# Performance work log

Hardware: AMD Instinct MI355X
Metric: run time of the kernel (lower is better)

## Reference

```python
import jax, jax.numpy as jnp
import numpy as np

B, H, C, HID, WIN, K = 8, 64, 128, 512, 4, 3
L = H * H

def _conv(x, w, groups, pad):
    return jax.lax.conv_general_dilated(
        x, w, (1, 1), [(pad, pad), (pad, pad)],
        dimension_numbers=('NCHW', 'OIHW', 'NCHW'), feature_group_count=groups)

def _ln(x, g, b):
    m = x.mean(-1, keepdims=True)
    v = ((x - m) ** 2).mean(-1, keepdims=True)
    return (x - m) * jax.lax.rsqrt(v + 1e-5) * g + b

def _gelu(x):
    return jax.nn.gelu(x, approximate=False)  # torch nn.GELU default = erf

def setup_inputs() -> dict:
    key = jax.random.key(0)
    ks = jax.random.split(key, 16)
    n = lambda i, sh: jax.random.normal(ks[i], sh, jnp.float32) * 0.02
    return dict(
        x=jax.random.normal(ks[0], (B, L, C), jnp.float32),
        ln1_g=jnp.ones((C,), jnp.float32), ln1_b=jnp.zeros((C,), jnp.float32),
        conv1_w=n(1, (WIN * C, C, K, K)),
        w_down=n(2, (WIN, C)), b_down=jnp.zeros((WIN,), jnp.float32),
        w1=n(3, (4 * WIN, WIN)), b1=jnp.zeros((4 * WIN,), jnp.float32),
        w2=n(4, (WIN, 4 * WIN)), b2=jnp.zeros((WIN,), jnp.float32),
        w_gk=n(5, (C, WIN * C)), b_gk=jnp.zeros((C,), jnp.float32),
        w_fus=n(6, (C, (WIN + 1) * C)), b_fus=jnp.zeros((C,), jnp.float32),
        ln2_g=jnp.ones((C,), jnp.float32), ln2_b=jnp.zeros((C,), jnp.float32),
        lin1_w=n(7, (HID, C)), lin1_b=jnp.zeros((HID,), jnp.float32),
        dw_w=n(8, (HID, 1, K, K)), dw_b=jnp.zeros((HID,), jnp.float32),
        lin2_w=n(9, (C, HID)), lin2_b=jnp.zeros((C,), jnp.float32),
    )

def _kernel_attn(x, conv1_w, w_down, b_down, w1, b1, w2, b2, w_gk, b_gk, w_fus, b_fus):
    ws = H // 2  # window grid is 2x2 since win_num=4
    xw = x.reshape(B, 2, ws, 2, ws, C).transpose(0, 1, 3, 5, 2, 4).reshape(B, WIN * C, ws, ws)
    wc = _conv(xw, conv1_w, WIN, 1)
    # WinKernel_Reweight (SE over windows)
    pooled = wc.mean((2, 3)).reshape(B, WIN, C)
    y = jnp.einsum('bgc,gc->bg', pooled, w_down) + b_down
    y = _gelu(y @ w1.T + b1)
    wgt = jax.nn.sigmoid(y @ w2.T + b2)
    k0 = conv1_w.reshape(WIN, C, C, K, K)
    kern = wgt[:, :, None, None, None, None] * k0[None]
    k_in = kern.transpose(0, 2, 1, 3, 4, 5).reshape(B * C, WIN * C, K, K)
    gk = jnp.einsum('om,nmij->noij', w_gk, k_in) + b_gk[None, :, None, None]
    kernels = jnp.concatenate([kern, gk.reshape(B, 1, C, C, K, K)], axis=1)
    kernels = kernels.reshape(B * (WIN + 1) * C, C, K, K)
    # per-sample dynamic grouped conv over full-resolution image
    ximg = x.reshape(B, H, H, C).transpose(0, 3, 1, 2)     # [B, C, H, W]
    xrep = jnp.tile(ximg, (1, WIN + 1, 1, 1)).reshape(1, B * (WIN + 1) * C, H, H)
    out = _conv(xrep, kernels, B * (WIN + 1), 1).reshape(B, (WIN + 1) * C, H, H)
    out = jnp.einsum('oc,bchw->bohw', w_fus, out) + b_fus[None, :, None, None]
    return out.transpose(0, 2, 3, 1).reshape(B, L, C)

def _leff(x, lin1_w, lin1_b, dw_w, dw_b, lin2_w, lin2_b):
    h = _gelu(x @ lin1_w.T + lin1_b)                       # [B, L, HID]
    h = h.reshape(B, H, H, HID).transpose(0, 3, 1, 2)
    h = _gelu(_conv(h, dw_w, HID, 1) + dw_b[None, :, None, None])  # depthwise 3x3
    h = h.transpose(0, 2, 3, 1).reshape(B, L, HID)
    return h @ lin2_w.T + lin2_b

def reference(x, ln1_g, ln1_b, conv1_w, w_down, b_down, w1, b1, w2, b2,
              w_gk, b_gk, w_fus, b_fus, ln2_g, ln2_b,
              lin1_w, lin1_b, dw_w, dw_b, lin2_w, lin2_b):
    x = x + _kernel_attn(_ln(x, ln1_g, ln1_b), conv1_w, w_down, b_down,
                         w1, b1, w2, b2, w_gk, b_gk, w_fus, b_fus)
    x = x + _leff(_ln(x, ln2_g, ln2_b), lin1_w, lin1_b, dw_w, dw_b, lin2_w, lin2_b)
    return x
```

## Files before the change

### kernel.cpp

```cpp
#include <hip/hip_runtime.h>
#include <math.h>

#define NB   8
#define HH   64
#define NC   128
#define NHID 512
#define NL   4096

typedef __attribute__((ext_vector_type(4))) float f32x4;
typedef __attribute__((ext_vector_type(8))) __bf16 bf16x8;

__device__ __forceinline__ float gelu_f(float v) {
  return 0.5f * v * (1.f + erff(v * 0.70710678118654752f));
}
__device__ __forceinline__ float sigmoid_f(float v) {
  return 1.f / (1.f + expf(-v));
}
__device__ __forceinline__ unsigned short f2bf(float f) {
  unsigned int u = __builtin_bit_cast(unsigned int, f);
  unsigned int r = (u + 0x7FFFu + ((u >> 16) & 1u)) >> 16;
  return (unsigned short)r;
}
__device__ __forceinline__ float bf2f(unsigned short h) {
  return __builtin_bit_cast(float, ((unsigned int)h) << 16);
}
__device__ __forceinline__ float bflo(unsigned int w) {
  return __builtin_bit_cast(float, w << 16);
}
__device__ __forceinline__ float bfhi(unsigned int w) {
  return __builtin_bit_cast(float, w & 0xFFFF0000u);
}
__device__ __forceinline__ void gld16(const void* g, void* l) {
  __builtin_amdgcn_global_load_lds(
      (const __attribute__((address_space(1))) unsigned int*)g,
      (__attribute__((address_space(3))) unsigned int*)l, 16, 0, 0);
}

template<bool SWZ>
__global__ __launch_bounds__(256) void ln_kernel(const float* __restrict__ x,
    const float* __restrict__ g, const float* __restrict__ bb, unsigned short* __restrict__ out) {
  int wv = threadIdx.x >> 6, l = threadIdx.x & 63;
  int row = blockIdx.x * 4 + wv;
  const float2 v = *(const float2*)(x + (size_t)row * NC + l * 2);
  float s = v.x + v.y, ss = v.x * v.x + v.y * v.y;
#pragma unroll
  for (int off = 32; off > 0; off >>= 1) {
    s  += __shfl_down(s, off);
    ss += __shfl_down(ss, off);
  }
  s = __shfl(s, 0); ss = __shfl(ss, 0);
  float mean = s * (1.f / NC);
  float rstd = rsqrtf(ss * (1.f / NC) - mean * mean + 1e-5f);
  const float2 gg = *(const float2*)(g + l * 2);
  const float2 bv = *(const float2*)(bb + l * 2);
  float o0 = (v.x - mean) * rstd * gg.x + bv.x;
  float o1 = (v.y - mean) * rstd * gg.y + bv.y;
  unsigned int pk = (unsigned int)f2bf(o0) | ((unsigned int)f2bf(o1) << 16);
  int c16 = l >> 2;
  int cs = SWZ ? (c16 ^ (row & 7)) : c16;
  *(unsigned int*)((char*)out + (size_t)row * 256 + (cs << 4) + (l & 3) * 4) = pk;
}

__global__ __launch_bounds__(128) void rs_kernel(const unsigned short* __restrict__ xln,
    float* __restrict__ RS) {
  int blk = blockIdx.x;
  int r = blk & 31, bw = blk >> 5;
  int win = bw & 3, b = bw >> 2;
  int hw = win >> 1, wn = win & 1;
  int cin = threadIdx.x;
  const unsigned short* base = xln + (((size_t)(b * 64 + hw * 32 + r)) * 64 + wn * 32) * NC + cin;
  float s = 0;
#pragma unroll
  for (int c = 0; c < 32; ++c) s += bf2f(base[(size_t)c * NC]);
  RS[(size_t)blk * 128 + cin] = s;
}

__global__ __launch_bounds__(128) void tfin_kernel(const unsigned short* __restrict__ xln,
    const float* __restrict__ RS, float* __restrict__ T) {
  int bw = blockIdx.x;
  int win = bw & 3, b = bw >> 2;
  int hw = win >> 1, wn = win & 1;
  int cin = threadIdx.x;
  const unsigned short* base = xln + (((size_t)(b * 64 + hw * 32)) * 64 + wn * 32) * NC + cin;
  float A = 0;
#pragma unroll
  for (int r = 0; r < 32; ++r) A += RS[(size_t)(bw * 32 + r) * 128 + cin];
  float r0  = RS[(size_t)(bw * 32) * 128 + cin];
  float r31 = RS[(size_t)(bw * 32 + 31) * 128 + cin];
  float c0 = 0, c31 = 0;
#pragma unroll
  for (int r = 0; r < 32; ++r) {
    c0  += bf2f(base[((size_t)r * 64) * NC]);
    c31 += bf2f(base[((size_t)r * 64 + 31) * NC]);
  }
  float x00 = bf2f(base[0]);
  float x0c = bf2f(base[(size_t)31 * NC]);
  float xr0 = bf2f(base[((size_t)31 * 64) * NC]);
  float xrc = bf2f(base[((size_t)31 * 64 + 31) * NC]);
  float* t = T + ((size_t)bw * 128 + cin) * 9;
  t[0] = A - r31 - c31 + xrc;
  t[1] = A - r31;
  t[2] = A - r31 - c0 + xr0;
  t[3] = A - c31;
  t[4] = A;
  t[5] = A - c0;
  t[6] = A - r0 - c31 + x0c;
  t[7] = A - r0;
  t[8] = A - r0 - c0 + x00;
}

__global__ __launch_bounds__(256) void se_kernel(const float* __restrict__ T,
    const float* __restrict__ U, const float* __restrict__ b_down,
    const float* __restrict__ w1, const float* __restrict__ b1,
    const float* __restrict__ w2, const float* __restrict__ b2, float* __restrict__ wgt) {
  __shared__ float ydot[32];
  int tid = threadIdx.x;
  int pair = tid >> 3, sub = tid & 7;
  int g = pair & 3;
  float acc = 0;
  for (int k = 0; k < 16; ++k) {
    int cin = sub * 16 + k;
    const float* tp = T + ((size_t)pair * 128 + cin) * 9;
#pragma unroll
    for (int ij = 0; ij < 9; ++ij)
      acc += U[(size_t)(g * 9 + ij) * 128 + cin] * tp[ij];
  }
#pragma unroll
  for (int off = 4; off > 0; off >>= 1) acc += __shfl_down(acc, off);
  if (sub == 0) ydot[pair] = acc;
  __syncthreads();
  if (tid < NB) {
    int b = tid;
    float y[4];
#pragma unroll
    for (int gg = 0; gg < 4; ++gg) y[gg] = ydot[b * 4 + gg] * (1.f / 1024.f) + b_down[gg];
    float y1[16];
#pragma unroll
    for (int i = 0; i < 16; ++i) {
      float a = b1[i];
#pragma unroll
      for (int gg = 0; gg < 4; ++gg) a += y[gg] * w1[i * 4 + gg];
      y1[i] = gelu_f(a);
    }
#pragma unroll
    for (int gg = 0; gg < 4; ++gg) {
      float a = b2[gg];
#pragma unroll
      for (int i = 0; i < 16; ++i) a += y1[i] * w2[gg * 16 + i];
      wgt[b * 4 + gg] = sigmoid_f(a);
    }
  }
}

__global__ __launch_bounds__(128) void prep_ct_kernel(const float* __restrict__ conv1_w,
    unsigned short* __restrict__ ctp, unsigned short* __restrict__ ctq) {
  int oc = blockIdx.x;
  int w = oc >> 7, c = oc & 127;
  int t = threadIdx.x;
  float v[9];
#pragma unroll
  for (int j = 0; j < 9; ++j) v[j] = conv1_w[(size_t)oc * 1152 + t * 9 + j];
#pragma unroll
  for (int j = 0; j < 9; ++j) {
    unsigned short bv = f2bf(v[j]);
    size_t prow = (size_t)(w * 9 + j) * 128 + c;
    *(unsigned short*)((char*)ctp + prow * 256 + ((((t >> 3) ^ (c & 7)) << 4) + (t & 7) * 2)) = bv;
    size_t qrow = (size_t)(w * 9 + j) * 128 + t;
    *(unsigned short*)((char*)ctq + qrow * 256 + ((((c >> 3) ^ (t & 7)) << 4) + (c & 7) * 2)) = bv;
  }
}

__global__ __launch_bounds__(256) void prep_misc_kernel(
    const float* __restrict__ lin1_w, const float* __restrict__ lin2_w,
    const float* __restrict__ w_gk, const float* __restrict__ w_fus,
    const float* __restrict__ dw_w,
    unsigned short* __restrict__ w1o, unsigned short* __restrict__ w2o,
    unsigned short* __restrict__ wgko, unsigned short* __restrict__ wf1o,
    unsigned short* __restrict__ wf2o, float* __restrict__ dwt,
    float* __restrict__ sfus) {
  int blk = blockIdx.x, tid = threadIdx.x;
  if (blk < 32) {
    int idx = blk * 256 + tid;
    int n = idx >> 4, c16 = idx & 15;
    const float4 a = *(const float4*)(lin1_w + (size_t)n * 128 + c16 * 8);
    const float4 b = *(const float4*)(lin1_w + (size_t)n * 128 + c16 * 8 + 4);
    unsigned int p0 = (unsigned int)f2bf(a.x) | ((unsigned int)f2bf(a.y) << 16);
    unsigned int p1 = (unsigned int)f2bf(a.z) | ((unsigned int)f2bf(a.w) << 16);
    unsigned int p2 = (unsigned int)f2bf(b.x) | ((unsigned int)f2bf(b.y) << 16);
    unsigned int p3 = (unsigned int)f2bf(b.z) | ((unsigned int)f2bf(b.w) << 16);
    *(uint4*)((char*)w1o + (size_t)n * 256 + ((c16 ^ (n & 7)) << 4)) = make_uint4(p0, p1, p2, p3);
  } else if (blk < 64) {
    int idx = (blk - 32) * 256 + tid;
    int kt = idx >> 11, c = (idx >> 4) & 127, c16 = idx & 15;
    const float* s = lin2_w + (size_t)c * NHID + kt * 128 + c16 * 8;
    const float4 a = *(const float4*)(s);
    const float4 b = *(const float4*)(s + 4);
    unsigned int p0 = (unsigned int)f2bf(a.x) | ((unsigned int)f2bf(a.y) << 16);
    unsigned int p1 = (unsigned int)f2bf(a.z) | ((unsigned int)f2bf(a.w) << 16);
    unsigned int p2 = (unsigned int)f2bf(b.x) | ((unsigned int)f2bf(b.y) << 16);
    unsigned int p3 = (unsigned int)f2bf(b.z) | ((unsigned int)f2bf(b.w) << 16);
    *(uint4*)((char*)w2o + (size_t)(kt * 128 + c) * 256 + ((c16 ^ (c & 7)) << 4)) = make_uint4(p0, p1, p2, p3);
  } else if (blk < 96) {
    int idx = (blk - 64) * 256 + tid;
    int row = idx >> 4, c16 = idx & 15;
    int w = row >> 7, q = row & 127;
    const float* s = w_gk + (size_t)q * 512 + w * 128 + c16 * 8;
    const float4 a = *(const float4*)(s);
    const float4 b = *(const float4*)(s + 4);
    unsigned int p0 = (unsigned int)f2bf(a.x) | ((unsigned int)f2bf(a.y) << 16);
    unsigned int p1 = (unsigned int)f2bf(a.z) | ((unsigned int)f2bf(a.w) << 16);
    unsigned int p2 = (unsigned int)f2bf(b.x) | ((unsigned int)f2bf(b.y) << 16);
    unsigned int p3 = (unsigned int)f2bf(b.z) | ((unsigned int)f2bf(b.w) << 16);
    *(uint4*)((char*)wgko + (size_t)row * 256 + ((c16 ^ (row & 7)) << 4)) = make_uint4(p0, p1, p2, p3);
  } else if (blk < 136) {
    int idx = (blk - 96) * 256 + tid;
    if (idx < 8192) {
      int row = idx >> 4, c16 = idx & 15;
      int w = row >> 7, o = row & 127;
      const float* s = w_fus + (size_t)o * 640 + w * 128 + c16 * 8;
      const float4 a = *(const float4*)(s);
      const float4 b = *(const float4*)(s + 4);
      unsigned int p0 = (unsigned int)f2bf(a.x) | ((unsigned int)f2bf(a.y) << 16);
      unsigned int p1 = (unsigned int)f2bf(a.z) | ((unsigned int)f2bf(a.w) << 16);
      unsigned int p2 = (unsigned int)f2bf(b.x) | ((unsigned int)f2bf(b.y) << 16);
      unsigned int p3 = (unsigned int)f2bf(b.z) | ((unsigned int)f2bf(b.w) << 16);
      *(uint4*)((char*)wf1o + (size_t)row * 256 + ((c16 ^ (row & 7)) << 4)) = make_uint4(p0, p1, p2, p3);
    } else if (idx < 10240) {
      int i2 = idx - 8192;
      int row = i2 >> 4, c16 = i2 & 15;
      const float* s = w_fus + (size_t)row * 640 + 512 + c16 * 8;
      const float4 a = *(const float4*)(s);
      const float4 b = *(const float4*)(s + 4);
      unsigned int p0 = (unsigned int)f2bf(a.x) | ((unsigned int)f2bf(a.y) << 16);
      unsigned int p1 = (unsigned int)f2bf(a.z) | ((unsigned int)f2bf(a.w) << 16);
      unsigned int p2 = (unsigned int)f2bf(b.x) | ((unsigned int)f2bf(b.y) << 16);
      unsigned int p3 = (unsigned int)f2bf(b.z) | ((unsigned int)f2bf(b.w) << 16);
      *(uint4*)((char*)wf2o + (size_t)row * 256 + ((c16 ^ (row & 7)) << 4)) = make_uint4(p0, p1, p2, p3);
    }
  } else if (blk < 154) {
    int idx = (blk - 136) * 256 + tid;
    if (idx < 4608) {
      int p = idx / 1152, rem = idx - p * 1152;
      int tap = rem >> 7, c = rem & 127;
      dwt[idx] = dw_w[(size_t)(p * 128 + c) * 9 + tap];
    }
  } else {
    if (tid < 128) {
      float s = 0;
      for (int p = 0; p < 128; ++p) s += w_fus[(size_t)tid * 640 + 512 + p];
      sfus[tid] = s;
    }
  }
}

__global__ __launch_bounds__(256) void gemmG_kernel(const unsigned short* __restrict__ Wgk,
    const unsigned short* __restrict__ CTP, const float* __restrict__ w_down,
    unsigned short* __restrict__ Gbf, float* __restrict__ U) {
  __shared__ uint4 LA[2048];
  __shared__ uint4 LB[2048];
  int bx = blockIdx.x;
  int w = bx / 9;
  int tid = threadIdx.x, wv = tid >> 6, l = tid & 63;
  const char* ga = (const char*)Wgk + (size_t)w * 32768;
  const char* gb = (const char*)CTP + (size_t)bx * 32768;
  for (int i = wv; i < 32; i += 4) gld16(ga + (i << 10) + l * 16, (char*)LA + (i << 10));
  for (int i = wv; i < 32; i += 4) gld16(gb + (i << 10) + l * 16, (char*)LB + (i << 10));
  __syncthreads();
  const f32x4 zero = {0.f, 0.f, 0.f, 0.f};
  f32x4 acc[2][8];
#pragma unroll
  for (int mt = 0; mt < 2; ++mt)
#pragma unroll
    for (int nt = 0; nt < 8; ++nt) acc[mt][nt] = zero;
  bf16x8 af[2][4];
#pragma unroll
  for (int mt = 0; mt < 2; ++mt) {
    int r = wv * 16 + mt * 64 + (l & 15);
#pragma unroll
    for (int ks = 0; ks < 4; ++ks) {
      int c16 = ks * 4 + (l >> 4);
      af[mt][ks] = *(const bf16x8*)((const char*)LA + r * 256 + ((c16 ^ (r & 7)) << 4));
    }
  }
#pragma unroll
  for (int nt = 0; nt < 8; ++nt) {
    int n = nt * 16 + (l & 15);
    bf16x8 bq[4];
#pragma unroll
    for (int ks = 0; ks < 4; ++ks) {
      int c16 = ks * 4 + (l >> 4);
      bq[ks] = *(const bf16x8*)((const char*)LB + n * 256 + ((c16 ^ (n & 7)) << 4));
    }
#pragma unroll
    for (int ks = 0; ks < 4; ++ks)
#pragma unroll
      for (int mt = 0; mt < 2; ++mt)
        acc[mt][nt] = __builtin_amdgcn_mfma_f32_16x16x32_bf16(af[mt][ks], bq[ks], acc[mt][nt], 0, 0, 0);
  }
  char* gout = (char*)Gbf + (size_t)bx * 32768;
#pragma unroll
  for (int mt = 0; mt < 2; ++mt)
#pragma unroll
    for (int nt = 0; nt < 8; ++nt) {
      int p = nt * 16 + (l & 15);
#pragma unroll
      for (int r2 = 0; r2 < 4; ++r2) {
        int q = wv * 16 + mt * 64 + (l >> 4) * 4 + r2;
        *(unsigned short*)(gout + q * 256 + ((((p >> 3) ^ (q & 7)) << 4) + (p & 7) * 2)) =
            f2bf(acc[mt][nt][r2]);
      }
    }
  if (tid < 128) {
    int cin = tid;
    int hi = cin >> 3, lo = (cin & 7) * 2;
    float s = 0;
    for (int cout = 0; cout < 128; ++cout) {
      unsigned short bv = *(const unsigned short*)((const char*)LB + cout * 256 +
                                                   (((hi ^ (cout & 7)) << 4) + lo));
      s += w_down[w * 128 + cout] * bf2f(bv);
    }
    U[(size_t)bx * 128 + cin] = s;
  }
}

__global__ __launch_bounds__(256) void gemmAW_kernel(const unsigned short* __restrict__ Wf1,
    const unsigned short* __restrict__ CTQ, const unsigned short* __restrict__ Wf2,
    const unsigned short* __restrict__ Gbf, float* __restrict__ AW) {
  __shared__ uint4 LA[2048];
  __shared__ uint4 LB[2048];
  int bx = blockIdx.x;
  int w = bx / 9;
  int tid = threadIdx.x, wv = tid >> 6, l = tid & 63;
  const f32x4 zero = {0.f, 0.f, 0.f, 0.f};
  f32x4 acc[2][8];
#pragma unroll
  for (int mt = 0; mt < 2; ++mt)
#pragma unroll
    for (int nt = 0; nt < 8; ++nt) acc[mt][nt] = zero;
  for (int ph = 0; ph < 2; ++ph) {
    if (ph) __syncthreads();
    const char* ga = ph ? (const char*)Wf2 : (const char*)Wf1 + (size_t)w * 32768;
    const char* gb = ph ? (const char*)Gbf + (size_t)bx * 32768
                        : (const char*)CTQ + (size_t)bx * 32768;
    for (int i = wv; i < 32; i += 4) gld16(ga + (i << 10) + l * 16, (char*)LA + (i << 10));
    for (int i = wv; i < 32; i += 4) gld16(gb + (i << 10) + l * 16, (char*)LB + (i << 10));
    __syncthreads();
    bf16x8 af[2][4];
#pragma unroll
    for (int mt = 0; mt < 2; ++mt) {
      int r = wv * 16 + mt * 64 + (l & 15);
#pragma unroll
      for (int ks = 0; ks < 4; ++ks) {
        int c16 = ks * 4 + (l >> 4);
        af[mt][ks] = *(const bf16x8*)((const char*)LA + r * 256 + ((c16 ^ (r & 7)) << 4));
      }
    }
#pragma unroll
    for (int nt = 0; nt < 8; ++nt) {
      int n = nt * 16 + (l & 15);
      bf16x8 bq[4];
#pragma unroll
      for (int ks = 0; ks < 4; ++ks) {
        int c16 = ks * 4 + (l >> 4);
        bq[ks] = *(const bf16x8*)((const char*)LB + n * 256 + ((c16 ^ (n & 7)) << 4));
      }
#pragma unroll
      for (int ks = 0; ks < 4; ++ks)
#pragma unroll
        for (int mt = 0; mt < 2; ++mt)
          acc[mt][nt] = __builtin_amdgcn_mfma_f32_16x16x32_bf16(af[mt][ks], bq[ks], acc[mt][nt], 0, 0, 0);
    }
  }
  float* aout = AW + (size_t)bx * 16384;
#pragma unroll
  for (int mt = 0; mt < 2; ++mt)
#pragma unroll
    for (int nt = 0; nt < 8; ++nt) {
      int q = nt * 16 + (l & 15);
#pragma unroll
      for (int r2 = 0; r2 < 4; ++r2) {
        int o = wv * 16 + mt * 64 + (l >> 4) * 4 + r2;
        aout[(size_t)o * 128 + q] = acc[mt][nt][r2];
      }
    }
}

__global__ __launch_bounds__(128) void m_kernel(const float* __restrict__ AW,
    const float* __restrict__ wgt, const float* __restrict__ sfus,
    const float* __restrict__ b_gk, unsigned short* __restrict__ Mb) {
  int blk = blockIdx.x;
  int b = blk >> 7;
  int o = blk & 127;
  int q = threadIdx.x;
  float a3 = sfus[o] * b_gk[q];
  float acc[9];
#pragma unroll
  for (int ij = 0; ij < 9; ++ij) acc[ij] = a3;
#pragma unroll
  for (int w = 0; w < 4; ++w) {
    float wv = wgt[b * 4 + w];
#pragma unroll
    for (int ij = 0; ij < 9; ++ij)
      acc[ij] += wv * AW[(((size_t)(w * 9 + ij) * 128 + o) * 128) + q];
  }
  int qswz = (q & 7) | (((q >> 3) ^ (o & 7)) << 3);
#pragma unroll
  for (int ij = 0; ij < 9; ++ij)
    Mb[(((size_t)(b * 9 + ij) * NC + o) * NC) + qswz] = f2bf(acc[ij]);
}

__global__ __launch_bounds__(256) void conv_kernel(const float* __restrict__ x0,
    const unsigned short* __restrict__ xln, const unsigned short* __restrict__ Mb,
    const float* __restrict__ b_fus, const float* __restrict__ ln2g,
    const float* __restrict__ ln2b, float* __restrict__ xout,
    unsigned short* __restrict__ xln2) {
  __shared__ uint4 XT[1600];
  __shared__ uint4 MT[2048];
  int bx = blockIdx.x;
  int b = bx >> 6, tile = bx & 63;
  int by = (tile >> 3) * 8, bxc = (tile & 7) * 8;
  int tid = threadIdx.x, wv = tid >> 6, l = tid & 63;
  for (int i = tid; i < 1600; i += 256) {
    int cell = i >> 4, c16 = i & 15;
    int pr = cell / 10, pc = cell - pr * 10;
    int gy = by + pr - 1, gx = bxc + pc - 1;
    uint4 v = make_uint4(0, 0, 0, 0);
    if ((unsigned)gy < 64u && (unsigned)gx < 64u)
      v = *(const uint4*)(xln + (((size_t)b * NL + gy * 64 + gx) * NC + c16 * 8));
    *(uint4*)((char*)XT + cell * 256 + ((c16 ^ (cell & 7)) << 4)) = v;
  }
  const char* mg = (const char*)Mb + (size_t)b * 9 * 32768;
  for (int i = wv; i < 32; i += 4) gld16(mg + (i << 10) + l * 16, (char*)MT + (i << 10));
  __syncthreads();

  const f32x4 zero = {0.f, 0.f, 0.f, 0.f};
  f32x4 acc[8];
#pragma unroll
  for (int nt = 0; nt < 8; ++nt) acc[nt] = zero;

  int sp = wv * 16 + (l & 15);
  int srow = sp >> 3, scol = sp & 7;

  for (int ij = 0; ij < 9; ++ij) {
    int di = ij / 3, dj = ij - di * 3;
    int cell = (srow + di) * 10 + scol + dj;
    bf16x8 af[4];
#pragma unroll
    for (int ks = 0; ks < 4; ++ks) {
      int c16 = ks * 4 + (l >> 4);
      af[ks] = *(const bf16x8*)((const char*)XT + cell * 256 + ((c16 ^ (cell & 7)) << 4));
    }
#pragma unroll
    for (int nt = 0; nt < 8; ++nt) {
      int oc = nt * 16 + (l & 15);
      bf16x8 bq[4];
#pragma unroll
      for (int ks = 0; ks < 4; ++ks) {
        int c16 = ks * 4 + (l >> 4);
        bq[ks] = *(const bf16x8*)((const char*)MT + oc * 256 + ((c16 ^ (oc & 7)) << 4));
      }
#pragma unroll
      for (int ks = 0; ks < 4; ++ks)
        acc[nt] = __builtin_amdgcn_mfma_f32_16x16x32_bf16(af[ks], bq[ks], acc[nt], 0, 0, 0);
    }
    __syncthreads();
    if (ij < 8) {
      const char* mg2 = mg + (size_t)(ij + 1) * 32768;
      for (int i = wv; i < 32; i += 4) gld16(mg2 + (i << 10) + l * 16, (char*)MT + (i << 10));
    }
    __syncthreads();
  }
  float s[4] = {0, 0, 0, 0}, ss2[4] = {0, 0, 0, 0};
  float vals[8][4];
#pragma unroll
  for (int nt = 0; nt < 8; ++nt) {
    int oc = nt * 16 + (l & 15);
    float bfv = b_fus[oc];
#pragma unroll
    for (int r2 = 0; r2 < 4; ++r2) {
      int sp2 = wv * 16 + (l >> 4) * 4 + r2;
      int gy = by + (sp2 >> 3), gx = bxc + (sp2 & 7);
      size_t gi = ((size_t)b * NL + gy * 64 + gx) * NC + oc;
      float v = x0[gi] + acc[nt][r2] + bfv;
      xout[gi] = v;
      vals[nt][r2] = v;
      s[r2] += v;
      ss2[r2] += v * v;
    }
  }
#pragma unroll
  for (int r2 = 0; r2 < 4; ++r2) {
#pragma unroll
    for (int off = 1; off < 16; off <<= 1) {
      s[r2]   += __shfl_xor(s[r2], off);
      ss2[r2] += __shfl_xor(ss2[r2], off);
    }
  }
  float mean[4], rstd[4];
#pragma unroll
  for (int r2 = 0; r2 < 4; ++r2) {
    mean[r2] = s[r2] * (1.f / 128.f);
    rstd[r2] = rsqrtf(ss2[r2] * (1.f / 128.f) - mean[r2] * mean[r2] + 1e-5f);
  }
#pragma unroll
  for (int nt = 0; nt < 8; ++nt) {
    int oc = nt * 16 + (l & 15);
    float gv = ln2g[oc], bv = ln2b[oc];
    int cc16 = oc >> 3, cby = (oc & 7) * 2;
#pragma unroll
    for (int r2 = 0; r2 < 4; ++r2) {
      int sp2 = wv * 16 + (l >> 4) * 4 + r2;
      int gy = by + (sp2 >> 3), gx = bxc + (sp2 & 7);
      size_t rowg = (size_t)b * NL + gy * 64 + gx;
      float o = (vals[nt][r2] - mean[r2]) * rstd[r2] * gv + bv;
      *(unsigned short*)((char*)xln2 + rowg * 256 + (((size_t)(cc16 ^ (int)(rowg & 7))) << 4) + cby) = f2bf(o);
    }
  }
}

__global__ __launch_bounds__(256) void lin1_kernel(const unsigned short* __restrict__ xa,
    const unsigned short* __restrict__ wb, const float* __restrict__ bias,
    unsigned short* __restrict__ h1p0, unsigned short* __restrict__ h1p123) {
  __shared__ uint4 XA[1024];
  __shared__ uint4 XB[2048];
  size_t rb = (size_t)blockIdx.x * 64;
  int tid = threadIdx.x, wv = tid >> 6, l = tid & 63;
  const char* ga = (const char*)xa + rb * 256;
  for (int i = wv; i < 16; i += 4) gld16(ga + (i << 10) + l * 16, (char*)XA + (i << 10));
  for (int i = wv; i < 32; i += 4) gld16((const char*)wb + (i << 10) + l * 16, (char*)XB + (i << 10));
  __syncthreads();
  int r = wv * 16 + (l & 15);
  bf16x8 af[4];
#pragma unroll
  for (int ks = 0; ks < 4; ++ks) {
    int c16 = ks * 4 + (l >> 4);
    af[ks] = *(const bf16x8*)((const char*)XA + r * 256 + ((c16 ^ (r & 7)) << 4));
  }
  const f32x4 zero = {0.f, 0.f, 0.f, 0.f};
  for (int cb = 0; cb < 4; ++cb) {
    f32x4 acc[8];
#pragma unroll
    for (int nt = 0; nt < 8; ++nt) acc[nt] = zero;
#pragma unroll
    for (int nt = 0; nt < 8; ++nt) {
      int n = nt * 16 + (l & 15);
      bf16x8 bq[4];
#pragma unroll
      for (int ks = 0; ks < 4; ++ks) {
        int c16 = ks * 4 + (l >> 4);
        bq[ks] = *(const bf16x8*)((const char*)XB + n * 256 + ((c16 ^ (n & 7)) << 4));
      }
#pragma unroll
      for (int ks = 0; ks < 4; ++ks)
        acc[nt] = __builtin_amdgcn_mfma_f32_16x16x32_bf16(af[ks], bq[ks], acc[nt], 0, 0, 0);
    }
    if (cb < 3) {
      __syncthreads();
      const char* gb = (const char*)wb + (size_t)(cb + 1) * 32768;
      for (int i = wv; i < 32; i += 4) gld16(gb + (i << 10) + l * 16, (char*)XB + (i << 10));
    }
    unsigned short* hp = (cb == 0) ? h1p0 : h1p123 + (size_t)(cb - 1) * 4194304;
#pragma unroll
    for (int nt = 0; nt < 8; ++nt) {
      int n = nt * 16 + (l & 15);
      float bsv = bias[cb * 128 + n];
#pragma unroll
      for (int r2 = 0; r2 < 4; ++r2) {
        size_t row = rb + wv * 16 + (l >> 4) * 4 + r2;
        hp[row * 128 + n] = f2bf(gelu_f(acc[nt][r2] + bsv));
      }
    }
    if (cb < 3) __syncthreads();
  }
}

__global__ __launch_bounds__(256) void dw_kernel(const unsigned short* __restrict__ h1p0,
    const unsigned short* __restrict__ h1p123, const float* __restrict__ dwt,
    const float* __restrict__ dw_b, unsigned short* __restrict__ h2p0,
    unsigned short* __restrict__ h2p123) {
  __shared__ unsigned char HT[6 * 64 * 128];
  __shared__ float wsm[9][64];
  int bx = blockIdx.x;
  int cp = bx >> 7;
  int rem = bx & 127;
  int bimg = rem >> 4, ys = rem & 15;
  int p = cp >> 1, chh = cp & 1;
  int y0 = ys * 4;
  int tid = threadIdx.x, wv = tid >> 6, l = tid & 63;
  const unsigned short* h1p = p ? h1p123 + (size_t)(p - 1) * 4194304 : h1p0;
  unsigned short* h2p = p ? h2p123 + (size_t)(p - 1) * 4194304 : h2p0;
  size_t ibase = (size_t)bimg * 4096;
  for (int i = tid; i < 576; i += 256)
    wsm[0][i] = dwt[(size_t)p * 1152 + (i >> 6) * 128 + chh * 64 + (i & 63)];
#pragma unroll
  for (int it = 0; it < 12; ++it) {
    int cb = it * 4 + wv;
    int row = cb >> 3, colblk = cb & 7;
    int yy = y0 - 1 + row;
    int ldsbase = (row * 64 + colblk * 8) * 128;
    if ((unsigned)yy < 64u) {
      const char* src = (const char*)h1p +
          (ibase + (size_t)yy * 64 + colblk * 8 + (l >> 3)) * 256 + chh * 128 + (l & 7) * 16;
      gld16(src, (char*)HT + ldsbase);
    } else {
      *(uint4*)((char*)HT + ldsbase + l * 16) = make_uint4(0, 0, 0, 0);
    }
  }
  int grp = tid >> 3, c8 = tid & 7;
  int ch0 = p * 128 + chh * 64 + c8 * 8;
  const float4 bs0 = *(const float4*)(dw_b + ch0);
  const float4 bs1 = *(const float4*)(dw_b + ch0 + 4);
  __syncthreads();

#pragma unroll
  for (int r = 0; r < 4; ++r) {
#pragma unroll
    for (int cc = 0; cc < 2; ++cc) {
      int col = grp * 2 + cc;
      float acw[8];
      acw[0] = bs0.x; acw[1] = bs0.y; acw[2] = bs0.z; acw[3] = bs0.w;
      acw[4] = bs1.x; acw[5] = bs1.y; acw[6] = bs1.z; acw[7] = bs1.w;
#pragma unroll
      for (int dy = 0; dy < 3; ++dy) {
#pragma unroll
        for (int dx = 0; dx < 3; ++dx) {
          int xc = col + dx - 1;
          if ((unsigned)xc < 64u) {
            const uint4 u = *(const uint4*)((const char*)HT +
                (((r + dy) * 64 + xc) * 128) + c8 * 16);
            const float4 wa  = *(const float4*)(&wsm[dy * 3 + dx][c8 * 8]);
            const float4 wb2 = *(const float4*)(&wsm[dy * 3 + dx][c8 * 8 + 4]);
            acw[0] += wa.x * bflo(u.x);  acw[1] += wa.y * bfhi(u.x);
            acw[2] += wa.z * bflo(u.y);  acw[3] += wa.w * bfhi(u.y);
            acw[4] += wb2.x * bflo(u.z); acw[5] += wb2.y * bfhi(u.z);
            acw[6] += wb2.z * bflo(u.w); acw[7] += wb2.w * bfhi(u.w);
          }
        }
      }
      size_t sidx = ibase + (size_t)(y0 + r) * 64 + col;
      int c16o = chh * 8 + c8;
      unsigned int o0 = (unsigned int)f2bf(gelu_f(acw[0])) | ((unsigned int)f2bf(gelu_f(acw[1])) << 16);
      unsigned int o1 = (unsigned int)f2bf(gelu_f(acw[2])) | ((unsigned int)f2bf(gelu_f(acw[3])) << 16);
      unsigned int o2 = (unsigned int)f2bf(gelu_f(acw[4])) | ((unsigned int)f2bf(gelu_f(acw[5])) << 16);
      unsigned int o3 = (unsigned int)f2bf(gelu_f(acw[6])) | ((unsigned int)f2bf(gelu_f(acw[7])) << 16);
      *(uint4*)(h2p + sidx * 128 + ((c16o ^ (int)(sidx & 7)) << 3)) = make_uint4(o0, o1, o2, o3);
    }
  }
}

__global__ __launch_bounds__(256) void lin2_kernel(const unsigned short* __restrict__ h2p0,
    const unsigned short* __restrict__ h2p123, const unsigned short* __restrict__ wb,
    const float* __restrict__ bias, const float* __restrict__ xres, float* __restrict__ out) {
  __shared__ uint4 XA[1024];
  __shared__ uint4 XB[2048];
  size_t rb = (size_t)blockIdx.x * 64;
  int tid = threadIdx.x, wv = tid >> 6, l = tid & 63;
  const f32x4 zero = {0.f, 0.f, 0.f, 0.f};
  f32x4 acc[8];
#pragma unroll
  for (int nt = 0; nt < 8; ++nt) acc[nt] = zero;
  int r = wv * 16 + (l & 15);
  for (int kt = 0; kt < 4; ++kt) {
    if (kt) __syncthreads();
    const unsigned short* hp = (kt == 0) ? h2p0 : h2p123 + (size_t)(kt - 1) * 4194304;
    const char* ga = (const char*)hp + rb * 256;
    const char* gb = (const char*)wb + (size_t)kt * 32768;
    for (int i = wv; i < 16; i += 4) gld16(ga + (i << 10) + l * 16, (char*)XA + (i << 10));
    for (int i = wv; i < 32; i += 4) gld16(gb + (i << 10) + l * 16, (char*)XB + (i << 10));
    __syncthreads();
    bf16x8 af[4];
#pragma unroll
    for (int ks = 0; ks < 4; ++ks) {
      int c16 = ks * 4 + (l >> 4);
      af[ks] = *(const bf16x8*)((const char*)XA + r * 256 + ((c16 ^ (r & 7)) << 4));
    }
#pragma unroll
    for (int nt = 0; nt < 8; ++nt) {
      int n = nt * 16 + (l & 15);
      bf16x8 bq[4];
#pragma unroll
      for (int ks = 0; ks < 4; ++ks) {
        int c16 = ks * 4 + (l >> 4);
        bq[ks] = *(const bf16x8*)((const char*)XB + n * 256 + ((c16 ^ (n & 7)) << 4));
      }
#pragma unroll
      for (int ks = 0; ks < 4; ++ks)
        acc[nt] = __builtin_amdgcn_mfma_f32_16x16x32_bf16(af[ks], bq[ks], acc[nt], 0, 0, 0);
    }
  }
#pragma unroll
  for (int nt = 0; nt < 8; ++nt) {
    int n = nt * 16 + (l & 15);
    float bsv = bias[n];
#pragma unroll
    for (int r2 = 0; r2 < 4; ++r2) {
      size_t row = rb + wv * 16 + (l >> 4) * 4 + r2;
      size_t gi = row * NC + n;
      out[gi] = xres[gi] + acc[nt][r2] + bsv;
    }
  }
}

extern "C" void kernel_launch(void* const* d_in, const int* in_sizes, int n_in,
                              void* d_out, int out_size, void* d_ws, size_t ws_size,
                              hipStream_t stream) {
  (void)in_sizes; (void)n_in; (void)out_size; (void)ws_size;
  const float* x       = (const float*)d_in[0];
  const float* ln1_g   = (const float*)d_in[1];
  const float* ln1_b   = (const float*)d_in[2];
  const float* conv1_w = (const float*)d_in[3];
  const float* w_down  = (const float*)d_in[4];
  const float* b_down  = (const float*)d_in[5];
  const float* w1      = (const float*)d_in[6];
  const float* b1      = (const float*)d_in[7];
  const float* w2      = (const float*)d_in[8];
  const float* b2      = (const float*)d_in[9];
  const float* w_gk    = (const float*)d_in[10];
  const float* b_gk    = (const float*)d_in[11];
  const float* w_fus   = (const float*)d_in[12];
  const float* b_fus   = (const float*)d_in[13];
  const float* ln2_g   = (const float*)d_in[14];
  const float* ln2_b   = (const float*)d_in[15];
  const float* lin1_w  = (const float*)d_in[16];
  const float* lin1_b  = (const float*)d_in[17];
  const float* dw_w    = (const float*)d_in[18];
  const float* dw_b    = (const float*)d_in[19];
  const float* lin2_w  = (const float*)d_in[20];
  const float* lin2_b  = (const float*)d_in[21];
  float* out = (float*)d_out;
  char* ws = (char*)d_ws;

  float*          xatt    = (float*)(ws);
  float*          Tb      = (float*)(ws + 16777216);
  float*          wgtb    = (float*)(ws + 16924672);
  float*          sfus    = (float*)(ws + 16925184);
  float*          dwt     = (float*)(ws + 16925696);
  unsigned short* Wgk_bf  = (unsigned short*)(ws + 16944128);
  unsigned short* Wf1_bf  = (unsigned short*)(ws + 17075200);
  unsigned short* Wf2_bf  = (unsigned short*)(ws + 17206272);
  unsigned short* w1_bf   = (unsigned short*)(ws + 17239040);
  unsigned short* w2_bf   = (unsigned short*)(ws + 17370112);
  unsigned short* M_bf    = (unsigned short*)(ws + 17501184);
  unsigned short* xln_bf  = (unsigned short*)(ws + 19860480);
  unsigned short* xln2_bf = (unsigned short*)(ws + 28249088);
  unsigned short* h1p123  = (unsigned short*)(ws + 36637696);
  unsigned short* h2p123  = (unsigned short*)(ws + 61803520);
  char* sc = ws + 28249088;
  float*          RSb     = (float*)(sc);
  float*          Ub      = (float*)(sc + 524288);
  unsigned short* CTP_bf  = (unsigned short*)(sc + 542720);
  unsigned short* CTQ_bf  = (unsigned short*)(sc + 1722368);
  unsigned short* G_bf    = (unsigned short*)(sc + 2902016);
  float*          AWb     = (float*)(sc + 4081664);

  ln_kernel<false><<<8192, 256, 0, stream>>>(x, ln1_g, ln1_b, xln_bf);
  prep_misc_kernel<<<155, 256, 0, stream>>>(lin1_w, lin2_w, w_gk, w_fus, dw_w,
                                            w1_bf, w2_bf, Wgk_bf, Wf1_bf, Wf2_bf, dwt, sfus);
  prep_ct_kernel<<<512, 128, 0, stream>>>(conv1_w, CTP_bf, CTQ_bf);
  rs_kernel<<<1024, 128, 0, stream>>>(xln_bf, RSb);
  gemmG_kernel<<<36, 256, 0, stream>>>(Wgk_bf, CTP_bf, w_down, G_bf, Ub);
  tfin_kernel<<<32, 128, 0, stream>>>(xln_bf, RSb, Tb);
  se_kernel<<<1, 256, 0, stream>>>(Tb, Ub, b_down, w1, b1, w2, b2, wgtb);
  gemmAW_kernel<<<36, 256, 0, stream>>>(Wf1_bf, CTQ_bf, Wf2_bf, G_bf, AWb);
  m_kernel<<<1024, 128, 0, stream>>>(AWb, wgtb, sfus, b_gk, M_bf);
  conv_kernel<<<512, 256, 0, stream>>>(x, xln_bf, M_bf, b_fus, ln2_g, ln2_b, xatt, xln2_bf);
  lin1_kernel<<<512, 256, 0, stream>>>(xln2_bf, w1_bf, lin1_b, xln_bf , h1p123);
  dw_kernel<<<1024, 256, 0, stream>>>(xln_bf , h1p123, dwt, dw_b,
                                      xln2_bf , h2p123);
  lin2_kernel<<<512, 256, 0, stream>>>(xln2_bf , h2p123, w2_bf, lin2_b, xatt, out);
}
```

Measured before the change: 163.8 us.

## Merge independent small kernels into combined launches to cut launch count

```diff
diff --git a/kernel.cpp b/kernel.cpp
--- a/kernel.cpp
+++ b/kernel.cpp
@@ -36,29 +36,119 @@
       (__attribute__((address_space(3))) unsigned int*)l, 16, 0, 0);
 }
 
-template<bool SWZ>
-__global__ __launch_bounds__(256) void ln_kernel(const float* __restrict__ x,
-    const float* __restrict__ g, const float* __restrict__ bb, unsigned short* __restrict__ out) {
-  int wv = threadIdx.x >> 6, l = threadIdx.x & 63;
-  int row = blockIdx.x * 4 + wv;
-  const float2 v = *(const float2*)(x + (size_t)row * NC + l * 2);
-  float s = v.x + v.y, ss = v.x * v.x + v.y * v.y;
-#pragma unroll
-  for (int off = 32; off > 0; off >>= 1) {
-    s  += __shfl_down(s, off);
-    ss += __shfl_down(ss, off);
-  }
-  s = __shfl(s, 0); ss = __shfl(ss, 0);
-  float mean = s * (1.f / NC);
-  float rstd = rsqrtf(ss * (1.f / NC) - mean * mean + 1e-5f);
-  const float2 gg = *(const float2*)(g + l * 2);
-  const float2 bv = *(const float2*)(bb + l * 2);
-  float o0 = (v.x - mean) * rstd * gg.x + bv.x;
-  float o1 = (v.y - mean) * rstd * gg.y + bv.y;
-  unsigned int pk = (unsigned int)f2bf(o0) | ((unsigned int)f2bf(o1) << 16);
-  int c16 = l >> 2;
-  int cs = SWZ ? (c16 ^ (row & 7)) : c16;
-  *(unsigned int*)((char*)out + (size_t)row * 256 + (cs << 4) + (l & 3) * 4) = pk;
+__device__ __forceinline__ void bf16x8_store(const float4& a, const float4& b, void* dst) {
+  unsigned int p0 = (unsigned int)f2bf(a.x) | ((unsigned int)f2bf(a.y) << 16);
+  unsigned int p1 = (unsigned int)f2bf(a.z) | ((unsigned int)f2bf(a.w) << 16);
+  unsigned int p2 = (unsigned int)f2bf(b.x) | ((unsigned int)f2bf(b.y) << 16);
+  unsigned int p3 = (unsigned int)f2bf(b.z) | ((unsigned int)f2bf(b.w) << 16);
+  *(uint4*)dst = make_uint4(p0, p1, p2, p3);
+}
+
+__global__ __launch_bounds__(256) void head_kernel(const float* __restrict__ x,
+    const float* __restrict__ ln1_g, const float* __restrict__ ln1_b,
+    unsigned short* __restrict__ xln,
+    const float* __restrict__ lin1_w, const float* __restrict__ lin2_w,
+    const float* __restrict__ w_gk, const float* __restrict__ w_fus,
+    const float* __restrict__ dw_w, const float* __restrict__ conv1_w,
+    unsigned short* __restrict__ w1o, unsigned short* __restrict__ w2o,
+    unsigned short* __restrict__ wgko, unsigned short* __restrict__ wf1o,
+    unsigned short* __restrict__ wf2o, float* __restrict__ dwt,
+    float* __restrict__ sfus,
+    unsigned short* __restrict__ ctp, unsigned short* __restrict__ ctq) {
+  int gblk = blockIdx.x, tid = threadIdx.x;
+  if (gblk < 8192) {
+    int wv = tid >> 6, l = tid & 63;
+    int row = gblk * 4 + wv;
+    const float2 v = *(const float2*)(x + (size_t)row * NC + l * 2);
+    float s = v.x + v.y, ss = v.x * v.x + v.y * v.y;
+#pragma unroll
+    for (int off = 32; off > 0; off >>= 1) {
+      s  += __shfl_down(s, off);
+      ss += __shfl_down(ss, off);
+    }
+    s = __shfl(s, 0); ss = __shfl(ss, 0);
+    float mean = s * (1.f / NC);
+    float rstd = rsqrtf(ss * (1.f / NC) - mean * mean + 1e-5f);
+    const float2 gg = *(const float2*)(ln1_g + l * 2);
+    const float2 bv = *(const float2*)(ln1_b + l * 2);
+    float o0 = (v.x - mean) * rstd * gg.x + bv.x;
+    float o1 = (v.y - mean) * rstd * gg.y + bv.y;
+    unsigned int pk = (unsigned int)f2bf(o0) | ((unsigned int)f2bf(o1) << 16);
+    *(unsigned int*)((char*)xln + (size_t)row * 256 + ((l >> 2) << 4) + (l & 3) * 4) = pk;
+    return;
+  }
+  if (gblk < 8347) {
+    int blk = gblk - 8192;
+    if (blk < 32) {
+      int idx = blk * 256 + tid;
+      int n = idx >> 4, c16 = idx & 15;
+      const float4 a = *(const float4*)(lin1_w + (size_t)n * 128 + c16 * 8);
+      const float4 b = *(const float4*)(lin1_w + (size_t)n * 128 + c16 * 8 + 4);
+      bf16x8_store(a, b, (char*)w1o + (size_t)n * 256 + ((c16 ^ (n & 7)) << 4));
+    } else if (blk < 64) {
+      int idx = (blk - 32) * 256 + tid;
+      int kt = idx >> 11, c = (idx >> 4) & 127, c16 = idx & 15;
+      const float* s = lin2_w + (size_t)c * NHID + kt * 128 + c16 * 8;
+      const float4 a = *(const float4*)(s);
+      const float4 b = *(const float4*)(s + 4);
+      bf16x8_store(a, b, (char*)w2o + (size_t)(kt * 128 + c) * 256 + ((c16 ^ (c & 7)) << 4));
+    } else if (blk < 96) {
+      int idx = (blk - 64) * 256 + tid;
+      int row = idx >> 4, c16 = idx & 15;
+      int w = row >> 7, q = row & 127;
+      const float* s = w_gk + (size_t)q * 512 + w * 128 + c16 * 8;
+      const float4 a = *(const float4*)(s);
+      const float4 b = *(const float4*)(s + 4);
+      bf16x8_store(a, b, (char*)wgko + (size_t)row * 256 + ((c16 ^ (row & 7)) << 4));
+    } else if (blk < 136) {
+      int idx = (blk - 96) * 256 + tid;
+      if (idx < 8192) {
+        int row = idx >> 4, c16 = idx & 15;
+        int w = row >> 7, o = row & 127;
+        const float* s = w_fus + (size_t)o * 640 + w * 128 + c16 * 8;
+        const float4 a = *(const float4*)(s);
+        const float4 b = *(const float4*)(s + 4);
+        bf16x8_store(a, b, (char*)wf1o + (size_t)row * 256 + ((c16 ^ (row & 7)) << 4));
+      } else if (idx < 10240) {
+        int i2 = idx - 8192;
+        int row = i2 >> 4, c16 = i2 & 15;
+        const float* s = w_fus + (size_t)row * 640 + 512 + c16 * 8;
+        const float4 a = *(const float4*)(s);
+        const float4 b = *(const float4*)(s + 4);
+        bf16x8_store(a, b, (char*)wf2o + (size_t)row * 256 + ((c16 ^ (row & 7)) << 4));
+      }
+    } else if (blk < 154) {
+      int idx = (blk - 136) * 256 + tid;
+      if (idx < 4608) {
+        int p = idx / 1152, rem = idx - p * 1152;
+        int tap = rem >> 7, c = rem & 127;
+        dwt[idx] = dw_w[(size_t)(p * 128 + c) * 9 + tap];
+      }
+    } else {
+      if (tid < 128) {
+        float s = 0;
+        for (int p = 0; p < 128; ++p) s += w_fus[(size_t)tid * 640 + 512 + p];
+        sfus[tid] = s;
+      }
+    }
+    return;
+  }
+  {
+    int oc = (gblk - 8347) * 2 + (tid >> 7);
+    int w = oc >> 7, c = oc & 127;
+    int t = tid & 127;
+    float v[9];
+#pragma unroll
+    for (int j = 0; j < 9; ++j) v[j] = conv1_w[(size_t)oc * 1152 + t * 9 + j];
+#pragma unroll
+    for (int j = 0; j < 9; ++j) {
+      unsigned short bv = f2bf(v[j]);
+      size_t prow = (size_t)(w * 9 + j) * 128 + c;
+      *(unsigned short*)((char*)ctp + prow * 256 + ((((t >> 3) ^ (c & 7)) << 4) + (t & 7) * 2)) = bv;
+      size_t qrow = (size_t)(w * 9 + j) * 128 + t;
+      *(unsigned short*)((char*)ctq + qrow * 256 + ((((c >> 3) ^ (t & 7)) << 4) + (c & 7) * 2)) = bv;
+    }
+  }
 }
 
 __global__ __launch_bounds__(128) void rs_kernel(const unsigned short* __restrict__ xln,
@@ -75,192 +165,52 @@
   RS[(size_t)blk * 128 + cin] = s;
 }
 
-__global__ __launch_bounds__(128) void tfin_kernel(const unsigned short* __restrict__ xln,
-    const float* __restrict__ RS, float* __restrict__ T) {
-  int bw = blockIdx.x;
-  int win = bw & 3, b = bw >> 2;
-  int hw = win >> 1, wn = win & 1;
-  int cin = threadIdx.x;
-  const unsigned short* base = xln + (((size_t)(b * 64 + hw * 32)) * 64 + wn * 32) * NC + cin;
-  float A = 0;
-#pragma unroll
-  for (int r = 0; r < 32; ++r) A += RS[(size_t)(bw * 32 + r) * 128 + cin];
-  float r0  = RS[(size_t)(bw * 32) * 128 + cin];
-  float r31 = RS[(size_t)(bw * 32 + 31) * 128 + cin];
-  float c0 = 0, c31 = 0;
-#pragma unroll
-  for (int r = 0; r < 32; ++r) {
-    c0  += bf2f(base[((size_t)r * 64) * NC]);
-    c31 += bf2f(base[((size_t)r * 64 + 31) * NC]);
-  }
-  float x00 = bf2f(base[0]);
-  float x0c = bf2f(base[(size_t)31 * NC]);
-  float xr0 = bf2f(base[((size_t)31 * 64) * NC]);
-  float xrc = bf2f(base[((size_t)31 * 64 + 31) * NC]);
-  float* t = T + ((size_t)bw * 128 + cin) * 9;
-  t[0] = A - r31 - c31 + xrc;
-  t[1] = A - r31;
-  t[2] = A - r31 - c0 + xr0;
-  t[3] = A - c31;
-  t[4] = A;
-  t[5] = A - c0;
-  t[6] = A - r0 - c31 + x0c;
-  t[7] = A - r0;
-  t[8] = A - r0 - c0 + x00;
-}
-
-__global__ __launch_bounds__(256) void se_kernel(const float* __restrict__ T,
-    const float* __restrict__ U, const float* __restrict__ b_down,
-    const float* __restrict__ w1, const float* __restrict__ b1,
-    const float* __restrict__ w2, const float* __restrict__ b2, float* __restrict__ wgt) {
-  __shared__ float ydot[32];
+__global__ __launch_bounds__(256) void gemmGT_kernel(const unsigned short* __restrict__ Wgk,
+    const unsigned short* __restrict__ CTP, const float* __restrict__ w_down,
+    unsigned short* __restrict__ Gbf, float* __restrict__ U,
+    const unsigned short* __restrict__ xln, const float* __restrict__ RS,
+    float* __restrict__ T) {
+  int gblk = blockIdx.x;
   int tid = threadIdx.x;
-  int pair = tid >> 3, sub = tid & 7;
-  int g = pair & 3;
-  float acc = 0;
-  for (int k = 0; k < 16; ++k) {
-    int cin = sub * 16 + k;
-    const float* tp = T + ((size_t)pair * 128 + cin) * 9;
-#pragma unroll
-    for (int ij = 0; ij < 9; ++ij)
-      acc += U[(size_t)(g * 9 + ij) * 128 + cin] * tp[ij];
-  }
-#pragma unroll
-  for (int off = 4; off > 0; off >>= 1) acc += __shfl_down(acc, off);
-  if (sub == 0) ydot[pair] = acc;
-  __syncthreads();
-  if (tid < NB) {
-    int b = tid;
-    float y[4];
-#pragma unroll
-    for (int gg = 0; gg < 4; ++gg) y[gg] = ydot[b * 4 + gg] * (1.f / 1024.f) + b_down[gg];
-    float y1[16];
-#pragma unroll
-    for (int i = 0; i < 16; ++i) {
-      float a = b1[i];
-#pragma unroll
-      for (int gg = 0; gg < 4; ++gg) a += y[gg] * w1[i * 4 + gg];
-      y1[i] = gelu_f(a);
-    }
-#pragma unroll
-    for (int gg = 0; gg < 4; ++gg) {
-      float a = b2[gg];
-#pragma unroll
-      for (int i = 0; i < 16; ++i) a += y1[i] * w2[gg * 16 + i];
-      wgt[b * 4 + gg] = sigmoid_f(a);
-    }
-  }
-}
-
-__global__ __launch_bounds__(128) void prep_ct_kernel(const float* __restrict__ conv1_w,
-    unsigned short* __restrict__ ctp, unsigned short* __restrict__ ctq) {
-  int oc = blockIdx.x;
-  int w = oc >> 7, c = oc & 127;
-  int t = threadIdx.x;
-  float v[9];
-#pragma unroll
-  for (int j = 0; j < 9; ++j) v[j] = conv1_w[(size_t)oc * 1152 + t * 9 + j];
-#pragma unroll
-  for (int j = 0; j < 9; ++j) {
-    unsigned short bv = f2bf(v[j]);
-    size_t prow = (size_t)(w * 9 + j) * 128 + c;
-    *(unsigned short*)((char*)ctp + prow * 256 + ((((t >> 3) ^ (c & 7)) << 4) + (t & 7) * 2)) = bv;
-    size_t qrow = (size_t)(w * 9 + j) * 128 + t;
-    *(unsigned short*)((char*)ctq + qrow * 256 + ((((c >> 3) ^ (t & 7)) << 4) + (c & 7) * 2)) = bv;
-  }
-}
-
-__global__ __launch_bounds__(256) void prep_misc_kernel(
-    const float* __restrict__ lin1_w, const float* __restrict__ lin2_w,
-    const float* __restrict__ w_gk, const float* __restrict__ w_fus,
-    const float* __restrict__ dw_w,
-    unsigned short* __restrict__ w1o, unsigned short* __restrict__ w2o,
-    unsigned short* __restrict__ wgko, unsigned short* __restrict__ wf1o,
-    unsigned short* __restrict__ wf2o, float* __restrict__ dwt,
-    float* __restrict__ sfus) {
-  int blk = blockIdx.x, tid = threadIdx.x;
-  if (blk < 32) {
-    int idx = blk * 256 + tid;
-    int n = idx >> 4, c16 = idx & 15;
-    const float4 a = *(const float4*)(lin1_w + (size_t)n * 128 + c16 * 8);
-    const float4 b = *(const float4*)(lin1_w + (size_t)n * 128 + c16 * 8 + 4);
-    unsigned int p0 = (unsigned int)f2bf(a.x) | ((unsigned int)f2bf(a.y) << 16);
-    unsigned int p1 = (unsigned int)f2bf(a.z) | ((unsigned int)f2bf(a.w) << 16);
-    unsigned int p2 = (unsigned int)f2bf(b.x) | ((unsigned int)f2bf(b.y) << 16);
-    unsigned int p3 = (unsigned int)f2bf(b.z) | ((unsigned int)f2bf(b.w) << 16);
-    *(uint4*)((char*)w1o + (size_t)n * 256 + ((c16 ^ (n & 7)) << 4)) = make_uint4(p0, p1, p2, p3);
-  } else if (blk < 64) {
-    int idx = (blk - 32) * 256 + tid;
-    int kt = idx >> 11, c = (idx >> 4) & 127, c16 = idx & 15;
-    const float* s = lin2_w + (size_t)c * NHID + kt * 128 + c16 * 8;
-    const float4 a = *(const float4*)(s);
-    const float4 b = *(const float4*)(s + 4);
-    unsigned int p0 = (unsigned int)f2bf(a.x) | ((unsigned int)f2bf(a.y) << 16);
-    unsigned int p1 = (unsigned int)f2bf(a.z) | ((unsigned int)f2bf(a.w) << 16);
-    unsigned int p2 = (unsigned int)f2bf(b.x) | ((unsigned int)f2bf(b.y) << 16);
-    unsigned int p3 = (unsigned int)f2bf(b.z) | ((unsigned int)f2bf(b.w) << 16);
-    *(uint4*)((char*)w2o + (size_t)(kt * 128 + c) * 256 + ((c16 ^ (c & 7)) << 4)) = make_uint4(p0, p1, p2, p3);
-  } else if (blk < 96) {
-    int idx = (blk - 64) * 256 + tid;
-    int row = idx >> 4, c16 = idx & 15;
-    int w = row >> 7, q = row & 127;
-    const float* s = w_gk + (size_t)q * 512 + w * 128 + c16 * 8;
-    const float4 a = *(const float4*)(s);
-    const float4 b = *(const float4*)(s + 4);
-    unsigned int p0 = (unsigned int)f2bf(a.x) | ((unsigned int)f2bf(a.y) << 16);
-    unsigned int p1 = (unsigned int)f2bf(a.z) | ((unsigned int)f2bf(a.w) << 16);
-    unsigned int p2 = (unsigned int)f2bf(b.x) | ((unsigned int)f2bf(b.y) << 16);
-    unsigned int p3 = (unsigned int)f2bf(b.z) | ((unsigned int)f2bf(b.w) << 16);
-    *(uint4*)((char*)wgko + (size_t)row * 256 + ((c16 ^ (row & 7)) << 4)) = make_uint4(p0, p1, p2, p3);
-  } else if (blk < 136) {
-    int idx = (blk - 96) * 256 + tid;
-    if (idx < 8192) {
-      int row = idx >> 4, c16 = idx & 15;
-      int w = row >> 7, o = row & 127;
-      const float* s = w_fus + (size_t)o * 640 + w * 128 + c16 * 8;
-      const float4 a = *(const float4*)(s);
-      const float4 b = *(const float4*)(s + 4);
-      unsigned int p0 = (unsigned int)f2bf(a.x) | ((unsigned int)f2bf(a.y) << 16);
-      unsigned int p1 = (unsigned int)f2bf(a.z) | ((unsigned int)f2bf(a.w) << 16);
-      unsigned int p2 = (unsigned int)f2bf(b.x) | ((unsigned int)f2bf(b.y) << 16);
-      unsigned int p3 = (unsigned int)f2bf(b.z) | ((unsigned int)f2bf(b.w) << 16);
-      *(uint4*)((char*)wf1o + (size_t)row * 256 + ((c16 ^ (row & 7)) << 4)) = make_uint4(p0, p1, p2, p3);
-    } else if (idx < 10240) {
-      int i2 = idx - 8192;
-      int row = i2 >> 4, c16 = i2 & 15;
-      const float* s = w_fus + (size_t)row * 640 + 512 + c16 * 8;
-      const float4 a = *(const float4*)(s);
-      const float4 b = *(const float4*)(s + 4);
-      unsigned int p0 = (unsigned int)f2bf(a.x) | ((unsigned int)f2bf(a.y) << 16);
-      unsigned int p1 = (unsigned int)f2bf(a.z) | ((unsigned int)f2bf(a.w) << 16);
-      unsigned int p2 = (unsigned int)f2bf(b.x) | ((unsigned int)f2bf(b.y) << 16);
-      unsigned int p3 = (unsigned int)f2bf(b.z) | ((unsigned int)f2bf(b.w) << 16);
-      *(uint4*)((char*)wf2o + (size_t)row * 256 + ((c16 ^ (row & 7)) << 4)) = make_uint4(p0, p1, p2, p3);
-    }
-  } else if (blk < 154) {
-    int idx = (blk - 136) * 256 + tid;
-    if (idx < 4608) {
-      int p = idx / 1152, rem = idx - p * 1152;
-      int tap = rem >> 7, c = rem & 127;
-      dwt[idx] = dw_w[(size_t)(p * 128 + c) * 9 + tap];
-    }
-  } else {
-    if (tid < 128) {
-      float s = 0;
-      for (int p = 0; p < 128; ++p) s += w_fus[(size_t)tid * 640 + 512 + p];
-      sfus[tid] = s;
-    }
-  }
-}
-
-__global__ __launch_bounds__(256) void gemmG_kernel(const unsigned short* __restrict__ Wgk,
-    const unsigned short* __restrict__ CTP, const float* __restrict__ w_down,
-    unsigned short* __restrict__ Gbf, float* __restrict__ U) {
+  if (gblk >= 36) {
+    if (tid >= 128) return;
+    int bw = gblk - 36;
+    int win = bw & 3, b = bw >> 2;
+    int hw = win >> 1, wn = win & 1;
+    int cin = tid;
+    const unsigned short* base = xln + (((size_t)(b * 64 + hw * 32)) * 64 + wn * 32) * NC + cin;
+    float A = 0;
+#pragma unroll
+    for (int r = 0; r < 32; ++r) A += RS[(size_t)(bw * 32 + r) * 128 + cin];
+    float r0  = RS[(size_t)(bw * 32) * 128 + cin];
+    float r31 = RS[(size_t)(bw * 32 + 31) * 128 + cin];
+    float c0 = 0, c31 = 0;
+#pragma unroll
+    for (int r = 0; r < 32; ++r) {
+      c0  += bf2f(base[((size_t)r * 64) * NC]);
+      c31 += bf2f(base[((size_t)r * 64 + 31) * NC]);
+    }
+    float x00 = bf2f(base[0]);
+    float x0c = bf2f(base[(size_t)31 * NC]);
+    float xr0 = bf2f(base[((size_t)31 * 64) * NC]);
+    float xrc = bf2f(base[((size_t)31 * 64 + 31) * NC]);
+    float* t = T + ((size_t)bw * 128 + cin) * 9;
+    t[0] = A - r31 - c31 + xrc;
+    t[1] = A - r31;
+    t[2] = A - r31 - c0 + xr0;
+    t[3] = A - c31;
+    t[4] = A;
+    t[5] = A - c0;
+    t[6] = A - r0 - c31 + x0c;
+    t[7] = A - r0;
+    t[8] = A - r0 - c0 + x00;
+    return;
+  }
   __shared__ uint4 LA[2048];
   __shared__ uint4 LB[2048];
-  int bx = blockIdx.x;
+  int bx = gblk;
   int w = bx / 9;
-  int tid = threadIdx.x, wv = tid >> 6, l = tid & 63;
+  int wv = tid >> 6, l = tid & 63;
   const char* ga = (const char*)Wgk + (size_t)w * 32768;
   const char* gb = (const char*)CTP + (size_t)bx * 32768;
   for (int i = wv; i < 32; i += 4) gld16(ga + (i << 10) + l * 16, (char*)LA + (i << 10));
@@ -323,14 +273,59 @@
   }
 }
 
-__global__ __launch_bounds__(256) void gemmAW_kernel(const unsigned short* __restrict__ Wf1,
+__global__ __launch_bounds__(256) void gemmAWse_kernel(const unsigned short* __restrict__ Wf1,
     const unsigned short* __restrict__ CTQ, const unsigned short* __restrict__ Wf2,
-    const unsigned short* __restrict__ Gbf, float* __restrict__ AW) {
+    const unsigned short* __restrict__ Gbf, float* __restrict__ AW,
+    const float* __restrict__ T, const float* __restrict__ U,
+    const float* __restrict__ b_down, const float* __restrict__ w1,
+    const float* __restrict__ b1, const float* __restrict__ w2,
+    const float* __restrict__ b2, float* __restrict__ wgt) {
   __shared__ uint4 LA[2048];
   __shared__ uint4 LB[2048];
-  int bx = blockIdx.x;
+  int gblk = blockIdx.x;
+  int tid = threadIdx.x;
+  if (gblk == 36) {
+    float* ydot = (float*)LA;
+    int pair = tid >> 3, sub = tid & 7;
+    int g = pair & 3;
+    float acc = 0;
+    for (int k = 0; k < 16; ++k) {
+      int cin = sub * 16 + k;
+      const float* tp = T + ((size_t)pair * 128 + cin) * 9;
+#pragma unroll
+      for (int ij = 0; ij < 9; ++ij)
+        acc += U[(size_t)(g * 9 + ij) * 128 + cin] * tp[ij];
+    }
+#pragma unroll
+    for (int off = 4; off > 0; off >>= 1) acc += __shfl_down(acc, off);
+    if (sub == 0) ydot[pair] = acc;
+    __syncthreads();
+    if (tid < NB) {
+      int b = tid;
+      float y[4];
+#pragma unroll
+      for (int gg = 0; gg < 4; ++gg) y[gg] = ydot[b * 4 + gg] * (1.f / 1024.f) + b_down[gg];
+      float y1[16];
+#pragma unroll
+      for (int i = 0; i < 16; ++i) {
+        float a = b1[i];
+#pragma unroll
+        for (int gg = 0; gg < 4; ++gg) a += y[gg] * w1[i * 4 + gg];
+        y1[i] = gelu_f(a);
+      }
+#pragma unroll
+      for (int gg = 0; gg < 4; ++gg) {
+        float a = b2[gg];
+#pragma unroll
+        for (int i = 0; i < 16; ++i) a += y1[i] * w2[gg * 16 + i];
+        wgt[b * 4 + gg] = sigmoid_f(a);
+      }
+    }
+    return;
+  }
+  int bx = gblk;
   int w = bx / 9;
-  int tid = threadIdx.x, wv = tid >> 6, l = tid & 63;
+  int wv = tid >> 6, l = tid & 63;
   const f32x4 zero = {0.f, 0.f, 0.f, 0.f};
   f32x4 acc[2][8];
 #pragma unroll
@@ -753,15 +748,15 @@
   unsigned short* G_bf    = (unsigned short*)(sc + 2902016);
   float*          AWb     = (float*)(sc + 4081664);
 
-  ln_kernel<false><<<8192, 256, 0, stream>>>(x, ln1_g, ln1_b, xln_bf);
-  prep_misc_kernel<<<155, 256, 0, stream>>>(lin1_w, lin2_w, w_gk, w_fus, dw_w,
-                                            w1_bf, w2_bf, Wgk_bf, Wf1_bf, Wf2_bf, dwt, sfus);
-  prep_ct_kernel<<<512, 128, 0, stream>>>(conv1_w, CTP_bf, CTQ_bf);
+  head_kernel<<<8603, 256, 0, stream>>>(x, ln1_g, ln1_b, xln_bf,
+                                        lin1_w, lin2_w, w_gk, w_fus, dw_w, conv1_w,
+                                        w1_bf, w2_bf, Wgk_bf, Wf1_bf, Wf2_bf, dwt, sfus,
+                                        CTP_bf, CTQ_bf);
   rs_kernel<<<1024, 128, 0, stream>>>(xln_bf, RSb);
-  gemmG_kernel<<<36, 256, 0, stream>>>(Wgk_bf, CTP_bf, w_down, G_bf, Ub);
-  tfin_kernel<<<32, 128, 0, stream>>>(xln_bf, RSb, Tb);
-  se_kernel<<<1, 256, 0, stream>>>(Tb, Ub, b_down, w1, b1, w2, b2, wgtb);
-  gemmAW_kernel<<<36, 256, 0, stream>>>(Wf1_bf, CTQ_bf, Wf2_bf, G_bf, AWb);
+  gemmGT_kernel<<<68, 256, 0, stream>>>(Wgk_bf, CTP_bf, w_down, G_bf, Ub,
+                                        xln_bf, RSb, Tb);
+  gemmAWse_kernel<<<37, 256, 0, stream>>>(Wf1_bf, CTQ_bf, Wf2_bf, G_bf, AWb,
+                                          Tb, Ub, b_down, w1, b1, w2, b2, wgtb);
   m_kernel<<<1024, 128, 0, stream>>>(AWb, wgtb, sfus, b_gk, M_bf);
   conv_kernel<<<512, 256, 0, stream>>>(x, xln_bf, M_bf, b_fus, ln2_g, ln2_b, xatt, xln2_bf);
   lin1_kernel<<<512, 256, 0, stream>>>(xln2_bf, w1_bf, lin1_b, xln_bf , h1p123);
```

Result: faster. 150.8 us (-8.0%).
